# Kernel tuning notes

Hardware: AMD Instinct MI355X
Metric: run time of the kernel (lower is better)

## Reference

```python
import jax, jax.numpy as jnp
import numpy as np

CHUNK = 256  # node-dim tile size; avoids materializing full (B,N,Din,Dout)


def setup_inputs() -> dict:
    key = jax.random.key(0)
    k1, k2 = jax.random.split(key)
    B, N, Din, Dout = 4, 8192, 128, 128
    x = jax.random.normal(k1, (B, N, Din), dtype=jnp.float32)
    W = jax.random.normal(k2, (Din, Dout), dtype=jnp.float32) * (1.0 / np.sqrt(Din))
    b = jnp.zeros((Dout,), dtype=jnp.float32)
    return {"x": x, "W": W, "b": b}


def reference(x, W, b):
    # x: (B, N, Din); gate = sigmoid(x @ W + b): (B, N, Dout)
    # gated = x[..., :, None] * gate[..., None, :]: (B, N, Din, Dout)
    # out = gated.max(axis=1).mean(axis=1): (B, Dout)
    B, N, Din = x.shape
    Dout = W.shape[1]
    n_chunks = N // CHUNK
    # (n_chunks, B, CHUNK, Din) so scan walks node tiles, keeping a running max
    xc = jnp.swapaxes(x.reshape(B, n_chunks, CHUNK, Din), 0, 1)

    def step(carry, xb):  # xb: (B, CHUNK, Din), carry: (B, Din, Dout)
        gate = jax.nn.sigmoid(jnp.einsum('bci,io->bco', xb, W) + b)  # (B,CHUNK,Dout)
        gated = xb[..., :, None] * gate[..., None, :]                # (B,CHUNK,Din,Dout)
        return jnp.maximum(carry, gated.max(axis=1)), None

    init = jnp.full((B, Din, Dout), -jnp.inf, dtype=x.dtype)
    pooled, _ = jax.lax.scan(step, init, xc)  # (B, Din, Dout)
    return pooled.mean(axis=1)  # (B, Dout)
```

## Files before the change

kernel.cpp:

```cpp
#include <hip/hip_runtime.h>
#include <math.h>

#define D 128
#define NNODES 8192
#define NBATCH 4

typedef _Float16 f16x8 __attribute__((ext_vector_type(8)));
typedef _Float16 f16x4 __attribute__((ext_vector_type(4)));
typedef _Float16 f16x2 __attribute__((ext_vector_type(2)));
typedef float f32x4 __attribute__((ext_vector_type(4)));

__device__ inline f16x2 bc(unsigned int v) { return __builtin_bit_cast(f16x2, v); }
__device__ inline unsigned int cb(f16x2 v) { return __builtin_bit_cast(unsigned int, v); }
__device__ inline f16x2 pkmax(f16x2 a, f16x2 b) {
    return __builtin_elementwise_max(a, b);
}
__device__ inline unsigned int fold2(unsigned int a) {
    return cb(pkmax(bc(a), bc(a >> 16))) & 0xFFFFu;
}

__global__ __launch_bounds__(256) void wfrag_kernel(
    const float* __restrict__ W, uint4* __restrict__ wfrag)
{
    int e    = blockIdx.x * 256 + threadIdx.x;
    int lane = e & 63, ks = (e >> 6) & 3, ot = e >> 8;
    int o  = ot * 16 + (lane & 15);
    int kb = ks * 32 + (lane >> 4) * 8;
    f16x8 f;
#pragma unroll
    for (int j = 0; j < 8; ++j) f[j] = (_Float16)W[(kb + j) * D + o];
    wfrag[e] = __builtin_bit_cast(uint4, f);
}

__global__ __launch_bounds__(256, 4) void fused_gate_pool(
    const float* __restrict__ x, const float* __restrict__ bias,
    const uint4* __restrict__ wfrag, uint2* __restrict__ slab)
{
    __shared__ _Float16     xA[32 * 136];
    __shared__ unsigned int xh2[16 * 128];
    __shared__ unsigned int gh2[16 * 128];

    const int t    = threadIdx.x;
    const int blk  = blockIdx.x;
    const size_t base = (size_t)blk * 32 * D;
    const int lane = t & 63, wave = t >> 6;
    const int stripe = wave & 1, oh = wave >> 1;
    const int quad = lane >> 4, col = lane & 15;

    const float4* xs4 = (const float4*)(x + base);
#pragma unroll
    for (int it = 0; it < 4; ++it) {
        int idx = t + 256 * it;
        int r = idx >> 5, c4 = idx & 31;
        float4 v = xs4[idx];
        f16x4 h = { (_Float16)v.x, (_Float16)v.y, (_Float16)v.z, (_Float16)v.w };
        *(f16x4*)&xA[r * 136 + c4 * 4] = h;
    }
#pragma unroll
    for (int it = 0; it < 2; ++it) {
        int idx = t + 256 * it;
        int p = idx >> 5, c4 = idx & 31;
        float4 a = xs4[(2 * p) * 32 + c4];
        float4 b = xs4[(2 * p + 1) * 32 + c4];
        uint4 u;
        u.x = cb((f16x2){(_Float16)a.x, (_Float16)b.x});
        u.y = cb((f16x2){(_Float16)a.y, (_Float16)b.y});
        u.z = cb((f16x2){(_Float16)a.z, (_Float16)b.z});
        u.w = cb((f16x2){(_Float16)a.w, (_Float16)b.w});
        *(uint4*)&xh2[p * 128 + c4 * 4] = u;
    }
    __syncthreads();

    f16x8 af[4];
#pragma unroll
    for (int ks = 0; ks < 4; ++ks)
        af[ks] = *(const f16x8*)&xA[(stripe * 16 + col) * 136 + ks * 32 + quad * 8];

    f32x4 acc[4];
#pragma unroll
    for (int ot = 0; ot < 4; ++ot) acc[ot] = (f32x4){0.f, 0.f, 0.f, 0.f};

#pragma unroll
    for (int ot = 0; ot < 4; ++ot) {
        uint4 bf[4];
#pragma unroll
        for (int ks = 0; ks < 4; ++ks)
            bf[ks] = wfrag[((oh * 4 + ot) * 4 + ks) * 64 + lane];
#pragma unroll
        for (int ks = 0; ks < 4; ++ks)
            acc[ot] = __builtin_amdgcn_mfma_f32_16x16x32_f16(
                af[ks], __builtin_bit_cast(f16x8, bf[ks]), acc[ot], 0, 0, 0);
    }

#pragma unroll
    for (int ot = 0; ot < 4; ++ot) {
        int o = oh * 64 + ot * 16 + col;
        float bv = bias[o];
#pragma unroll
        for (int rr = 0; rr < 2; ++rr) {
            float g0 = 1.0f / (1.0f + __expf(-(acc[ot][2 * rr]     + bv)));
            float g1 = 1.0f / (1.0f + __expf(-(acc[ot][2 * rr + 1] + bv)));
            gh2[(stripe * 8 + quad * 2 + rr) * 128 + o] =
                cb((f16x2){(_Float16)g0, (_Float16)g1});
        }
    }
    __syncthreads();

    const int ti = t >> 4;
    const int to = t & 15;
    const f16x2 NEGINF = bc(0xFC00FC00u);

    f16x2 pa[8][8];
#pragma unroll
    for (int ii = 0; ii < 8; ++ii)
#pragma unroll
        for (int oo = 0; oo < 8; ++oo) pa[ii][oo] = NEGINF;

    const unsigned int* xpi = &xh2[ti * 4];
    const unsigned int* gpi = &gh2[to * 4];
#pragma unroll
    for (int p = 0; p < 16; ++p) {
        uint4 xa = *(const uint4*)&xpi[p * 128];
        uint4 xb = *(const uint4*)&xpi[p * 128 + 64];
        uint4 ga = *(const uint4*)&gpi[p * 128];
        uint4 gb = *(const uint4*)&gpi[p * 128 + 64];
        f16x2 xv[8] = {bc(xa.x), bc(xa.y), bc(xa.z), bc(xa.w),
                       bc(xb.x), bc(xb.y), bc(xb.z), bc(xb.w)};
        f16x2 gv[8] = {bc(ga.x), bc(ga.y), bc(ga.z), bc(ga.w),
                       bc(gb.x), bc(gb.y), bc(gb.z), bc(gb.w)};
#pragma unroll
        for (int ii = 0; ii < 8; ++ii)
#pragma unroll
            for (int oo = 0; oo < 8; ++oo)
                pa[ii][oo] = pkmax(pa[ii][oo], xv[ii] * gv[oo]);
    }

    uint2* sd = slab + (size_t)blk * 4096;
#pragma unroll
    for (int ii = 0; ii < 8; ++ii) {
        int ip = (ii < 4) ? (ti * 4 + ii) : (64 + ti * 4 + (ii - 4));
        unsigned int a[8];
#pragma unroll
        for (int oo = 0; oo < 8; ++oo) a[oo] = cb(pa[ii][oo]);
        unsigned int r01 = fold2(a[0]) | (fold2(a[1]) << 16);
        unsigned int r23 = fold2(a[2]) | (fold2(a[3]) << 16);
        unsigned int r45 = fold2(a[4]) | (fold2(a[5]) << 16);
        unsigned int r67 = fold2(a[6]) | (fold2(a[7]) << 16);
        uint2 v0 = {r01, r23};
        uint2 v1 = {r45, r67};
        sd[ip * 32 + to]      = v0;
        sd[ip * 32 + 16 + to] = v1;
    }
}

__global__ __launch_bounds__(256) void reduce_kernel(
    const unsigned int* __restrict__ slab, float* __restrict__ out)
{
    __shared__ unsigned int red[3][64];
    const int rb = blockIdx.x;
    const int b  = rb >> 7, i = rb & 127;
    const int t  = threadIdx.x;
    const int og = t & 63, sg = t >> 6;

    const unsigned int* p =
        slab + (size_t)(b * 256 + sg * 64) * 8192 + i * 64 + og;
    f16x2 m = bc(0xFC00FC00u);
#pragma unroll 8
    for (int it = 0; it < 64; ++it)
        m = pkmax(m, bc(p[(size_t)it * 8192]));

    if (sg) red[sg - 1][og] = cb(m);
    __syncthreads();
    if (sg == 0) {
        m = pkmax(m, bc(red[0][og]));
        m = pkmax(m, bc(red[1][og]));
        m = pkmax(m, bc(red[2][og]));
        atomicAdd(&out[b * D + og * 2],     (float)m[0] * 0.0078125f);
        atomicAdd(&out[b * D + og * 2 + 1], (float)m[1] * 0.0078125f);
    }
}

extern "C" void kernel_launch(void* const* d_in, const int* in_sizes, int n_in,
                              void* d_out, int out_size, void* d_ws, size_t ws_size,
                              hipStream_t stream)
{
    const float* x    = (const float*)d_in[0];
    const float* W    = (const float*)d_in[1];
    const float* bias = (const float*)d_in[2];
    float* out = (float*)d_out;

    uint4* wfrag = (uint4*)d_ws;
    uint2* slab  = (uint2*)((char*)d_ws + 65536);

    (void)hipMemsetAsync(d_out, 0, (size_t)out_size * sizeof(float), stream);
    wfrag_kernel<<<8, 256, 0, stream>>>(W, wfrag);
    fused_gate_pool<<<1024, 256, 0, stream>>>(x, bias, wfrag, slab);
    reduce_kernel<<<512, 256, 0, stream>>>((const unsigned int*)slab, out);
}
```

Before: 104.9 us.

## Process 64 nodes per block and build MFMA A-fragments from packed pair layout

Each block now handles 64 nodes instead of 32, which halves the grid and halves the per-block partial-max slab that the reduce kernel must scan. The separate fp16 row buffer for the MFMA A operand is dropped. A fragments are instead rebuilt from the node-pair-packed buffer with byte permutes, and each wave computes all 128 outputs while prefetching the next W fragments. Rows are padded to 132 words to reduce LDS bank conflicts. The trade-off is longer per-block work, more accumulator registers and fewer blocks to spread across the CUs.

```diff
diff --git a/kernel.cpp b/kernel.cpp
--- a/kernel.cpp
+++ b/kernel.cpp
@@ -4,9 +4,9 @@
 #define D 128
 #define NNODES 8192
 #define NBATCH 4
+#define RW 132
 
 typedef _Float16 f16x8 __attribute__((ext_vector_type(8)));
-typedef _Float16 f16x4 __attribute__((ext_vector_type(4)));
 typedef _Float16 f16x2 __attribute__((ext_vector_type(2)));
 typedef float f32x4 __attribute__((ext_vector_type(4)));
 
@@ -36,28 +36,18 @@
     const float* __restrict__ x, const float* __restrict__ bias,
     const uint4* __restrict__ wfrag, uint2* __restrict__ slab)
 {
-    __shared__ _Float16     xA[32 * 136];
-    __shared__ unsigned int xh2[16 * 128];
-    __shared__ unsigned int gh2[16 * 128];
+    __shared__ unsigned int xh2[32 * RW];
+    __shared__ unsigned int gh2[32 * RW];
 
     const int t    = threadIdx.x;
     const int blk  = blockIdx.x;
-    const size_t base = (size_t)blk * 32 * D;
+    const size_t base = (size_t)blk * 64 * D;
     const int lane = t & 63, wave = t >> 6;
-    const int stripe = wave & 1, oh = wave >> 1;
     const int quad = lane >> 4, col = lane & 15;
 
     const float4* xs4 = (const float4*)(x + base);
 #pragma unroll
     for (int it = 0; it < 4; ++it) {
-        int idx = t + 256 * it;
-        int r = idx >> 5, c4 = idx & 31;
-        float4 v = xs4[idx];
-        f16x4 h = { (_Float16)v.x, (_Float16)v.y, (_Float16)v.z, (_Float16)v.w };
-        *(f16x4*)&xA[r * 136 + c4 * 4] = h;
-    }
-#pragma unroll
-    for (int it = 0; it < 2; ++it) {
         int idx = t + 256 * it;
         int p = idx >> 5, c4 = idx & 31;
         float4 a = xs4[(2 * p) * 32 + c4];
@@ -67,40 +57,59 @@
         u.y = cb((f16x2){(_Float16)a.y, (_Float16)b.y});
         u.z = cb((f16x2){(_Float16)a.z, (_Float16)b.z});
         u.w = cb((f16x2){(_Float16)a.w, (_Float16)b.w});
-        *(uint4*)&xh2[p * 128 + c4 * 4] = u;
+        *(uint4*)&xh2[p * RW + c4 * 4] = u;
     }
     __syncthreads();
 
+    const unsigned int sel = (col & 1) ? 0x07060302u : 0x05040100u;
+    const int prow = wave * 8 + (col >> 1);
+
     f16x8 af[4];
 #pragma unroll
-    for (int ks = 0; ks < 4; ++ks)
-        af[ks] = *(const f16x8*)&xA[(stripe * 16 + col) * 136 + ks * 32 + quad * 8];
-
-    f32x4 acc[4];
-#pragma unroll
-    for (int ot = 0; ot < 4; ++ot) acc[ot] = (f32x4){0.f, 0.f, 0.f, 0.f};
-
-#pragma unroll
-    for (int ot = 0; ot < 4; ++ot) {
-        uint4 bf[4];
-#pragma unroll
-        for (int ks = 0; ks < 4; ++ks)
-            bf[ks] = wfrag[((oh * 4 + ot) * 4 + ks) * 64 + lane];
+    for (int ks = 0; ks < 4; ++ks) {
+        int kb = ks * 32 + quad * 8;
+        uint4 u0 = *(const uint4*)&xh2[prow * RW + kb];
+        uint4 u1 = *(const uint4*)&xh2[prow * RW + kb + 4];
+        uint4 r;
+        r.x = __builtin_amdgcn_perm(u0.y, u0.x, sel);
+        r.y = __builtin_amdgcn_perm(u0.w, u0.z, sel);
+        r.z = __builtin_amdgcn_perm(u1.y, u1.x, sel);
+        r.w = __builtin_amdgcn_perm(u1.w, u1.z, sel);
+        af[ks] = __builtin_bit_cast(f16x8, r);
+    }
+
+    f32x4 acc[8];
+#pragma unroll
+    for (int ot = 0; ot < 8; ++ot) acc[ot] = (f32x4){0.f, 0.f, 0.f, 0.f};
+
+    uint4 bf[4];
+#pragma unroll
+    for (int ks = 0; ks < 4; ++ks) bf[ks] = wfrag[ks * 64 + lane];
+#pragma unroll
+    for (int ot = 0; ot < 8; ++ot) {
+        uint4 cur[4];
+#pragma unroll
+        for (int ks = 0; ks < 4; ++ks) cur[ks] = bf[ks];
+        if (ot < 7) {
+#pragma unroll
+            for (int ks = 0; ks < 4; ++ks)
+                bf[ks] = wfrag[((ot + 1) * 4 + ks) * 64 + lane];
+        }
 #pragma unroll
         for (int ks = 0; ks < 4; ++ks)
             acc[ot] = __builtin_amdgcn_mfma_f32_16x16x32_f16(
-                af[ks], __builtin_bit_cast(f16x8, bf[ks]), acc[ot], 0, 0, 0);
-    }
-
-#pragma unroll
-    for (int ot = 0; ot < 4; ++ot) {
-        int o = oh * 64 + ot * 16 + col;
+                af[ks], __builtin_bit_cast(f16x8, cur[ks]), acc[ot], 0, 0, 0);
+    }
+
+#pragma unroll
+    for (int ot = 0; ot < 8; ++ot) {
+        int o = ot * 16 + col;
         float bv = bias[o];
 #pragma unroll
         for (int rr = 0; rr < 2; ++rr) {
             float g0 = 1.0f / (1.0f + __expf(-(acc[ot][2 * rr]     + bv)));
             float g1 = 1.0f / (1.0f + __expf(-(acc[ot][2 * rr + 1] + bv)));
-            gh2[(stripe * 8 + quad * 2 + rr) * 128 + o] =
+            gh2[(wave * 8 + quad * 2 + rr) * RW + o] =
                 cb((f16x2){(_Float16)g0, (_Float16)g1});
         }
     }
@@ -108,22 +117,21 @@
 
     const int ti = t >> 4;
     const int to = t & 15;
-    const f16x2 NEGINF = bc(0xFC00FC00u);
 
     f16x2 pa[8][8];
 #pragma unroll
     for (int ii = 0; ii < 8; ++ii)
 #pragma unroll
-        for (int oo = 0; oo < 8; ++oo) pa[ii][oo] = NEGINF;
+        for (int oo = 0; oo < 8; ++oo) pa[ii][oo] = bc(0xFC00FC00u);
 
     const unsigned int* xpi = &xh2[ti * 4];
     const unsigned int* gpi = &gh2[to * 4];
 #pragma unroll
-    for (int p = 0; p < 16; ++p) {
-        uint4 xa = *(const uint4*)&xpi[p * 128];
-        uint4 xb = *(const uint4*)&xpi[p * 128 + 64];
-        uint4 ga = *(const uint4*)&gpi[p * 128];
-        uint4 gb = *(const uint4*)&gpi[p * 128 + 64];
+    for (int p = 0; p < 32; ++p) {
+        uint4 xa = *(const uint4*)&xpi[p * RW];
+        uint4 xb = *(const uint4*)&xpi[p * RW + 64];
+        uint4 ga = *(const uint4*)&gpi[p * RW];
+        uint4 gb = *(const uint4*)&gpi[p * RW + 64];
         f16x2 xv[8] = {bc(xa.x), bc(xa.y), bc(xa.z), bc(xa.w),
                        bc(xb.x), bc(xb.y), bc(xb.z), bc(xb.w)};
         f16x2 gv[8] = {bc(ga.x), bc(ga.y), bc(ga.z), bc(ga.w),
@@ -163,10 +171,10 @@
     const int og = t & 63, sg = t >> 6;
 
     const unsigned int* p =
-        slab + (size_t)(b * 256 + sg * 64) * 8192 + i * 64 + og;
+        slab + (size_t)(b * 128 + sg * 32) * 8192 + i * 64 + og;
     f16x2 m = bc(0xFC00FC00u);
 #pragma unroll 8
-    for (int it = 0; it < 64; ++it)
+    for (int it = 0; it < 32; ++it)
         m = pkmax(m, bc(p[(size_t)it * 8192]));
 
     if (sg) red[sg - 1][og] = cb(m);
@@ -194,6 +202,6 @@
 
     (void)hipMemsetAsync(d_out, 0, (size_t)out_size * sizeof(float), stream);
     wfrag_kernel<<<8, 256, 0, stream>>>(W, wfrag);
-    fused_gate_pool<<<1024, 256, 0, stream>>>(x, bias, wfrag, slab);
+    fused_gate_pool<<<512, 256, 0, stream>>>(x, bias, wfrag, slab);
     reduce_kernel<<<512, 256, 0, stream>>>((const unsigned int*)slab, out);
 }
```

Result: faster. 101.9 us (-2.8%).
